# Kernel optimization log

Hardware: AMD Instinct MI355X
Metric: run time of the kernel (lower is better)

Reference implementation:

```python
import jax, jax.numpy as jnp
import numpy as np

NUM_CAPS = 10
DIM_CAPS = 16
ROUTINGS = 3


def setup_inputs() -> dict:
    key = jax.random.key(0)
    k1, k2 = jax.random.split(key)
    x = jax.random.normal(k1, (128, 1152, 512), dtype=jnp.float32)
    # glorot-uniform-ish scale for W [D_in, num_caps*dim_caps]
    limit = (6.0 / (512 + NUM_CAPS * DIM_CAPS)) ** 0.5
    W = jax.random.uniform(k2, (512, NUM_CAPS * DIM_CAPS), dtype=jnp.float32,
                           minval=-limit, maxval=limit)
    return {"x": x, "W": W}


def _squash(s, axis=-1):
    # s_norm = ||s|| + 1e-7; out = s_norm^2/(1+s_norm^2) * s/s_norm
    s_norm = jnp.linalg.norm(s, axis=axis, keepdims=True) + 1e-7
    return (s_norm ** 2) / (1.0 + s_norm ** 2) * (s / s_norm)


def reference(x, W):
    B, N, _ = x.shape
    # u_hat: [B, N, C, D]
    u_hat = jnp.matmul(x, W).reshape(B, N, NUM_CAPS, DIM_CAPS)
    b = jnp.zeros((B, N, NUM_CAPS), dtype=u_hat.dtype)
    v = None
    for i in range(ROUTINGS):
        c = jax.nn.softmax(b, axis=2)                      # [B, N, C]
        s = jnp.einsum('bnc,bncd->bcd', c, u_hat)          # [B, C, D]
        v = _squash(s)                                     # [B, C, D]
        if i < ROUTINGS - 1:
            b = b + jnp.einsum('bncd,bcd->bnc', u_hat, v)
    return v
```

## Files before the change

### kernel.cpp

```cpp
#include <hip/hip_runtime.h>

#define BB 128
#define NN 1152
#define KD 512
#define NC 10
#define ND 16
#define CD 160

typedef unsigned short ushort_t;
typedef unsigned int uint_t;
typedef short short8v __attribute__((ext_vector_type(8)));
typedef float float4v __attribute__((ext_vector_type(4)));

__device__ __forceinline__ float bf2f(ushort_t u) {
  return __uint_as_float(((uint_t)u) << 16);
}
__device__ __forceinline__ ushort_t f2bf(float f) {
  uint_t x = __float_as_uint(f);
  x += 0x7fffu + ((x >> 16) & 1u);
  return (ushort_t)(x >> 16);
}

#define BAR_LDS() do {                                   \
    __builtin_amdgcn_sched_barrier(0);                   \
    asm volatile("s_waitcnt lgkmcnt(0)" ::: "memory");   \
    __builtin_amdgcn_s_barrier();                        \
    __builtin_amdgcn_sched_barrier(0);                   \
  } while (0)

__global__ __launch_bounds__(256) void wconv(const float* __restrict__ W,
                                             ushort_t* __restrict__ Wt) {
  int idx = blockIdx.x * 256 + threadIdx.x;
  int n = idx >> 9, k = idx & 511;
  Wt[idx] = f2bf(W[(size_t)k * CD + n]);
}

__global__ __launch_bounds__(256) void gemm_mfma(
    const float* __restrict__ x, const ushort_t* __restrict__ Wt,
    ushort_t* __restrict__ uhat, float* __restrict__ partials) {
  __shared__ char smem[57344];
  __shared__ float sA[4][CD];
  const int tid = threadIdx.x;
  const int wave = tid >> 6, lane = tid & 63;
  const int lrow = lane & 15, lg = lane >> 4;
  const int row0 = blockIdx.x * 64;

  float4v acc[10];
#pragma unroll
  for (int nt = 0; nt < 10; ++nt)
#pragma unroll
    for (int r = 0; r < 4; ++r) acc[nt][r] = 0.f;

  const int arow_ = tid >> 3;
  const int as = tid & 7;
  int bsrc[5], bby[5];
#pragma unroll
  for (int i = 0; i < 5; ++i) {
    int f = tid + i * 256;
    int br = f >> 3, bs = f & 7;
    bsrc[i] = br * KD + bs * 8;
    bby[i] = ((br << 7) + (bs << 4)) ^ ((br & 7) << 4);
  }
  const int aby0 = ((arow_ << 7) + (as << 4)) ^ ((arow_ & 7) << 4);
  const int aby1 = (((arow_ + 32) << 7) + (as << 4)) ^ (((arow_ + 32) & 7) << 4);

  float4v rA[2][2];
  short8v rB[5];

  auto LOADS = [&](int ks) {
    int k0 = ks * 64;
#pragma unroll
    for (int i = 0; i < 2; ++i) {
      const float* p = x + (size_t)(row0 + arow_ + i * 32) * KD + k0 + as * 8;
      rA[i][0] = *reinterpret_cast<const float4v*>(p);
      rA[i][1] = *reinterpret_cast<const float4v*>(p + 4);
    }
#pragma unroll
    for (int i = 0; i < 5; ++i)
      rB[i] = *reinterpret_cast<const short8v*>(Wt + bsrc[i] + k0);
  };
  auto WRITES = [&](int buf) {
    char* Ab = smem + buf * 8192;
    char* Bb = smem + 16384 + buf * 20480;
#pragma unroll
    for (int i = 0; i < 2; ++i) {
      short8v pk;
#pragma unroll
      for (int e = 0; e < 4; ++e) {
        pk[e] = (short)f2bf(rA[i][0][e]);
        pk[e + 4] = (short)f2bf(rA[i][1][e]);
      }
      *reinterpret_cast<short8v*>(Ab + (i ? aby1 : aby0)) = pk;
    }
#pragma unroll
    for (int i = 0; i < 5; ++i)
      *reinterpret_cast<short8v*>(Bb + bby[i]) = rB[i];
  };

  const int arow = wave * 16 + lrow;
  LOADS(0);
  WRITES(0);
  LOADS(1);
  BAR_LDS();
  int cur = 0;
  for (int ks = 0; ks < 8; ++ks) {
    const char* Ab = smem + cur * 8192;
    const char* Bb = smem + 16384 + cur * 20480;
#pragma unroll
    for (int kk = 0; kk < 2; ++kk) {
      int abyte = ((arow << 7) + kk * 64 + lg * 16) ^ ((arow & 7) << 4);
      short8v a = *reinterpret_cast<const short8v*>(Ab + abyte);
#pragma unroll
      for (int nt = 0; nt < 10; ++nt) {
        int brow = nt * 16 + lrow;
        int bbyte = ((brow << 7) + kk * 64 + lg * 16) ^ ((brow & 7) << 4);
        short8v bfr = *reinterpret_cast<const short8v*>(Bb + bbyte);
        acc[nt] = __builtin_amdgcn_mfma_f32_16x16x32_bf16(a, bfr, acc[nt], 0, 0, 0);
      }
    }
    if (ks < 7) {
      WRITES(cur ^ 1);
      if (ks < 6) LOADS(ks + 2);
    }
    BAR_LDS();
    cur ^= 1;
  }

#pragma unroll
  for (int nt = 0; nt < 10; ++nt) {
    float p = acc[nt][0] + acc[nt][1] + acc[nt][2] + acc[nt][3];
    p += __shfl_xor(p, 16);
    p += __shfl_xor(p, 32);
    if (lg == 0) sA[wave][nt * 16 + lrow] = p;
  }

  ushort_t* Ct = reinterpret_cast<ushort_t*>(smem);
#pragma unroll
  for (int nt = 0; nt < 10; ++nt)
#pragma unroll
    for (int r = 0; r < 4; ++r) {
      int row = wave * 16 + lg * 4 + r;
      Ct[row * 168 + nt * 16 + lrow] = f2bf(acc[nt][r]);
    }
  __syncthreads();
  if (tid < CD) {
    float s = sA[0][tid] + sA[1][tid] + sA[2][tid] + sA[3][tid];
    partials[(size_t)blockIdx.x * CD + tid] = s;
  }
#pragma unroll
  for (int i = 0; i < 5; ++i) {
    int p = tid + i * 256;
    int row = p / 20, c0 = (p % 20) * 8;
    *reinterpret_cast<short8v*>(&uhat[(size_t)(row0 + row) * CD + c0]) =
        *reinterpret_cast<const short8v*>(&Ct[row * 168 + c0]);
  }
}

#define ITER_T 640
template <int ITER2>
__global__ __launch_bounds__(ITER_T) void iter_k(
    const ushort_t* __restrict__ uhat, const float* __restrict__ pg,
    const float* __restrict__ p1, float* __restrict__ pout) {
  __shared__ float bv[128][NC];
  __shared__ float wv[128][NC];
  __shared__ float sred[32][CD];
  __shared__ float sred2[4][CD];
  __shared__ float vv[CD];
  const int blk = blockIdx.x;
  const int b = blk / 9, ch = blk % 9;
  const int t = threadIdx.x;
  const int g = t / 20, q = t % 20;
  const int c = q >> 1;
  const ushort_t* ub = uhat + ((size_t)b * NN + ch * 128) * CD + q * 8;

  if (t < CD) {
    float s0 = 0.f;
#pragma unroll
    for (int cc = 0; cc < 18; ++cc) s0 += pg[((size_t)b * 18 + cc) * CD + t];
    s0 *= 0.1f;
    float ss = s0 * s0;
    ss += __shfl_xor(ss, 1); ss += __shfl_xor(ss, 2);
    ss += __shfl_xor(ss, 4); ss += __shfl_xor(ss, 8);
    float sn = sqrtf(ss) + 1e-7f;
    float v = s0 * sn / (1.f + sn * sn);
    if (ITER2) {
      float s1 = 0.f;
#pragma unroll
      for (int cc = 0; cc < 9; ++cc) s1 += p1[((size_t)b * 9 + cc) * CD + t];
      float ss1 = s1 * s1;
      ss1 += __shfl_xor(ss1, 1); ss1 += __shfl_xor(ss1, 2);
      ss1 += __shfl_xor(ss1, 4); ss1 += __shfl_xor(ss1, 8);
      float sn1 = sqrtf(ss1) + 1e-7f;
      v += s1 * sn1 / (1.f + sn1 * sn1);
    }
    vv[t] = v;
  }
  __syncthreads();

  float v0r[8];
  {
    float4v a = *reinterpret_cast<const float4v*>(&vv[q * 8]);
    float4v bb = *reinterpret_cast<const float4v*>(&vv[q * 8 + 4]);
#pragma unroll
    for (int e = 0; e < 4; ++e) { v0r[e] = a[e]; v0r[e + 4] = bb[e]; }
  }

  short8v u8[4];
#pragma unroll
  for (int it = 0; it < 4; ++it) {
    int n = g + it * 32;
    u8[it] = *reinterpret_cast<const short8v*>(ub + (size_t)n * CD);
    float p = 0.f;
#pragma unroll
    for (int e = 0; e < 8; ++e) p += bf2f((ushort_t)u8[it][e]) * v0r[e];
    p += __shfl_xor(p, 1);
    if ((q & 1) == 0) bv[n][c] = p;
  }
  __syncthreads();

  if (t < 128) {
    float e[NC];
    float bm = bv[t][0];
#pragma unroll
    for (int cc = 1; cc < NC; ++cc) bm = fmaxf(bm, bv[t][cc]);
    float Z = 0.f;
#pragma unroll
    for (int cc = 0; cc < NC; ++cc) { e[cc] = __expf(bv[t][cc] - bm); Z += e[cc]; }
    float rz = 1.f / Z;
#pragma unroll
    for (int cc = 0; cc < NC; ++cc) wv[t][cc] = e[cc] * rz;
  }
  __syncthreads();

  float a[8];
#pragma unroll
  for (int e = 0; e < 8; ++e) a[e] = 0.f;
#pragma unroll
  for (int it = 0; it < 4; ++it) {
    int n = g + it * 32;
    float w = wv[n][c];
#pragma unroll
    for (int e = 0; e < 8; ++e) a[e] += w * bf2f((ushort_t)u8[it][e]);
  }
  {
    float4v lo, hi;
#pragma unroll
    for (int e = 0; e < 4; ++e) { lo[e] = a[e]; hi[e] = a[e + 4]; }
    float4v* dst = reinterpret_cast<float4v*>(&sred[g][q * 8]);
    dst[0] = lo; dst[1] = hi;
  }
  __syncthreads();
  {
    int col = t % CD, part = t / CD;
    float s = 0.f;
#pragma unroll
    for (int g8 = 0; g8 < 8; ++g8) s += sred[part * 8 + g8][col];
    sred2[part][col] = s;
  }
  __syncthreads();
  if (t < CD) {
    pout[(size_t)blk * CD + t] =
        sred2[0][t] + sred2[1][t] + sred2[2][t] + sred2[3][t];
  }
}

__global__ __launch_bounds__(CD) void squash_out(
    const float* __restrict__ p2, float* __restrict__ outp) {
  int b = blockIdx.x, t = threadIdx.x;
  float s = 0.f;
#pragma unroll
  for (int cc = 0; cc < 9; ++cc) s += p2[((size_t)b * 9 + cc) * CD + t];
  float ss = s * s;
  ss += __shfl_xor(ss, 1); ss += __shfl_xor(ss, 2);
  ss += __shfl_xor(ss, 4); ss += __shfl_xor(ss, 8);
  float sn = sqrtf(ss) + 1e-7f;
  outp[(size_t)b * CD + t] = s * sn / (1.f + sn * sn);
}

extern "C" void kernel_launch(void* const* d_in, const int* in_sizes, int n_in,
                              void* d_out, int out_size, void* d_ws, size_t ws_size,
                              hipStream_t stream) {
  const float* x = (const float*)d_in[0];
  const float* W = (const float*)d_in[1];
  float* out = (float*)d_out;

  char* ws = (char*)d_ws;
  ushort_t* uhat = (ushort_t*)ws;
  ushort_t* Wt   = (ushort_t*)(ws + 47185920);
  float*    pg   = (float*)(ws + 47185920 + 163840);
  float*    p1   = (float*)(ws + 48824320);
  float*    p2   = (float*)(ws + 49561600);

  wconv<<<320, 256, 0, stream>>>(W, Wt);
  gemm_mfma<<<2304, 256, 0, stream>>>(x, Wt, uhat, pg);
  iter_k<0><<<1152, ITER_T, 0, stream>>>(uhat, pg, nullptr, p1);
  iter_k<1><<<1152, ITER_T, 0, stream>>>(uhat, pg, p1, p2);
  squash_out<<<BB, CD, 0, stream>>>(p2, out);
}
```

Baseline: 109.8 us.

## Halve GEMM K-tile to shrink LDS and raise occupancy

The GEMM K-step drops from 64 to 32, so each of the 16 iterations loads one A row-chunk per thread and up to three B chunks. LDS falls from about 57KB to 28KB, the swizzle is rewritten for 64-byte rows, and the row-sum scratch now reuses the main buffer. Launch bounds ask for 4 blocks per CU. The aim is more resident blocks to hide global load latency, paid for with twice as many barriers and less work between them.

```diff
diff --git a/kernel.cpp b/kernel.cpp
--- a/kernel.cpp
+++ b/kernel.cpp
@@ -35,11 +35,10 @@
   Wt[idx] = f2bf(W[(size_t)k * CD + n]);
 }
 
-__global__ __launch_bounds__(256) void gemm_mfma(
+__global__ __launch_bounds__(256, 4) void gemm_mfma(
     const float* __restrict__ x, const ushort_t* __restrict__ Wt,
     ushort_t* __restrict__ uhat, float* __restrict__ partials) {
-  __shared__ char smem[57344];
-  __shared__ float sA[4][CD];
+  __shared__ __align__(16) char smem[28672];
   const int tid = threadIdx.x;
   const int wave = tid >> 6, lane = tid & 63;
   const int lrow = lane & 15, lg = lane >> 4;
@@ -51,87 +50,79 @@
 #pragma unroll
     for (int r = 0; r < 4; ++r) acc[nt][r] = 0.f;
 
-  const int arow_ = tid >> 3;
-  const int as = tid & 7;
-  int bsrc[5], bby[5];
-#pragma unroll
-  for (int i = 0; i < 5; ++i) {
+  const int arow_ = tid >> 2;
+  const int as = tid & 3;
+  const int aby = (arow_ << 6) + ((as ^ ((arow_ >> 1) & 3)) << 4);
+  int bsrc[3], bby[3];
+#pragma unroll
+  for (int i = 0; i < 3; ++i) {
     int f = tid + i * 256;
-    int br = f >> 3, bs = f & 7;
+    int br = f >> 2, bs = f & 3;
     bsrc[i] = br * KD + bs * 8;
-    bby[i] = ((br << 7) + (bs << 4)) ^ ((br & 7) << 4);
-  }
-  const int aby0 = ((arow_ << 7) + (as << 4)) ^ ((arow_ & 7) << 4);
-  const int aby1 = (((arow_ + 32) << 7) + (as << 4)) ^ (((arow_ + 32) & 7) << 4);
-
-  float4v rA[2][2];
-  short8v rB[5];
+    bby[i] = (br << 6) + ((bs ^ ((br >> 1) & 3)) << 4);
+  }
+  const bool b2ok = (tid + 512) < 640;
+
+  float4v rA[2];
+  short8v rB[3];
 
   auto LOADS = [&](int ks) {
-    int k0 = ks * 64;
-#pragma unroll
-    for (int i = 0; i < 2; ++i) {
-      const float* p = x + (size_t)(row0 + arow_ + i * 32) * KD + k0 + as * 8;
-      rA[i][0] = *reinterpret_cast<const float4v*>(p);
-      rA[i][1] = *reinterpret_cast<const float4v*>(p + 4);
-    }
-#pragma unroll
-    for (int i = 0; i < 5; ++i)
-      rB[i] = *reinterpret_cast<const short8v*>(Wt + bsrc[i] + k0);
+    int k0 = ks * 32;
+    const float* p = x + (size_t)(row0 + arow_) * KD + k0 + as * 8;
+    rA[0] = *reinterpret_cast<const float4v*>(p);
+    rA[1] = *reinterpret_cast<const float4v*>(p + 4);
+    rB[0] = *reinterpret_cast<const short8v*>(Wt + bsrc[0] + k0);
+    rB[1] = *reinterpret_cast<const short8v*>(Wt + bsrc[1] + k0);
+    if (b2ok) rB[2] = *reinterpret_cast<const short8v*>(Wt + bsrc[2] + k0);
   };
   auto WRITES = [&](int buf) {
-    char* Ab = smem + buf * 8192;
-    char* Bb = smem + 16384 + buf * 20480;
-#pragma unroll
-    for (int i = 0; i < 2; ++i) {
-      short8v pk;
-#pragma unroll
-      for (int e = 0; e < 4; ++e) {
-        pk[e] = (short)f2bf(rA[i][0][e]);
-        pk[e + 4] = (short)f2bf(rA[i][1][e]);
-      }
-      *reinterpret_cast<short8v*>(Ab + (i ? aby1 : aby0)) = pk;
-    }
-#pragma unroll
-    for (int i = 0; i < 5; ++i)
-      *reinterpret_cast<short8v*>(Bb + bby[i]) = rB[i];
+    char* Ab = smem + buf * 4096;
+    char* Bb = smem + 8192 + buf * 10240;
+    short8v pk;
+#pragma unroll
+    for (int e = 0; e < 4; ++e) {
+      pk[e] = (short)f2bf(rA[0][e]);
+      pk[e + 4] = (short)f2bf(rA[1][e]);
+    }
+    *reinterpret_cast<short8v*>(Ab + aby) = pk;
+    *reinterpret_cast<short8v*>(Bb + bby[0]) = rB[0];
+    *reinterpret_cast<short8v*>(Bb + bby[1]) = rB[1];
+    if (b2ok) *reinterpret_cast<short8v*>(Bb + bby[2]) = rB[2];
   };
 
   const int arow = wave * 16 + lrow;
+  const int afrag_by = (arow << 6) + ((lg ^ ((arow >> 1) & 3)) << 4);
   LOADS(0);
   WRITES(0);
   LOADS(1);
   BAR_LDS();
   int cur = 0;
-  for (int ks = 0; ks < 8; ++ks) {
-    const char* Ab = smem + cur * 8192;
-    const char* Bb = smem + 16384 + cur * 20480;
-#pragma unroll
-    for (int kk = 0; kk < 2; ++kk) {
-      int abyte = ((arow << 7) + kk * 64 + lg * 16) ^ ((arow & 7) << 4);
-      short8v a = *reinterpret_cast<const short8v*>(Ab + abyte);
-#pragma unroll
-      for (int nt = 0; nt < 10; ++nt) {
-        int brow = nt * 16 + lrow;
-        int bbyte = ((brow << 7) + kk * 64 + lg * 16) ^ ((brow & 7) << 4);
-        short8v bfr = *reinterpret_cast<const short8v*>(Bb + bbyte);
-        acc[nt] = __builtin_amdgcn_mfma_f32_16x16x32_bf16(a, bfr, acc[nt], 0, 0, 0);
-      }
-    }
-    if (ks < 7) {
+  for (int ks = 0; ks < 16; ++ks) {
+    const char* Ab = smem + cur * 4096;
+    const char* Bb = smem + 8192 + cur * 10240;
+    short8v a = *reinterpret_cast<const short8v*>(Ab + afrag_by);
+#pragma unroll
+    for (int nt = 0; nt < 10; ++nt) {
+      int brow = nt * 16 + lrow;
+      int bbyte = (brow << 6) + ((lg ^ ((brow >> 1) & 3)) << 4);
+      short8v bfr = *reinterpret_cast<const short8v*>(Bb + bbyte);
+      acc[nt] = __builtin_amdgcn_mfma_f32_16x16x32_bf16(a, bfr, acc[nt], 0, 0, 0);
+    }
+    if (ks < 15) {
       WRITES(cur ^ 1);
-      if (ks < 6) LOADS(ks + 2);
+      if (ks < 14) LOADS(ks + 2);
     }
     BAR_LDS();
     cur ^= 1;
   }
 
+  float* sAf = reinterpret_cast<float*>(smem + 24576);
 #pragma unroll
   for (int nt = 0; nt < 10; ++nt) {
     float p = acc[nt][0] + acc[nt][1] + acc[nt][2] + acc[nt][3];
     p += __shfl_xor(p, 16);
     p += __shfl_xor(p, 32);
-    if (lg == 0) sA[wave][nt * 16 + lrow] = p;
+    if (lg == 0) sAf[wave * CD + nt * 16 + lrow] = p;
   }
 
   ushort_t* Ct = reinterpret_cast<ushort_t*>(smem);
@@ -144,7 +135,7 @@
     }
   __syncthreads();
   if (tid < CD) {
-    float s = sA[0][tid] + sA[1][tid] + sA[2][tid] + sA[3][tid];
+    float s = sAf[tid] + sAf[CD + tid] + sAf[2 * CD + tid] + sAf[3 * CD + tid];
     partials[(size_t)blockIdx.x * CD + tid] = s;
   }
 #pragma unroll
```

Result: slower. 123.3 us (+12.3%).

## Double GEMM row tile to 128 with 512-thread blocks sharing W tile

Applied to the files above, without the earlier changes.

The GEMM block now covers 128 rows of x with 8 waves instead of 64 rows with 4, so each staged W tile in LDS is reused by twice as many rows. This halves the grid and halves the per-block partial sums, and the iteration kernel now reduces 9 partials per batch instead of 18. LDS per block grows to about 77KB, which can limit how many blocks fit per CU, and the larger block may change latency hiding.

```diff
diff --git a/kernel.cpp b/kernel.cpp
--- a/kernel.cpp
+++ b/kernel.cpp
@@ -35,15 +35,14 @@
   Wt[idx] = f2bf(W[(size_t)k * CD + n]);
 }
 
-__global__ __launch_bounds__(256) void gemm_mfma(
+__global__ __launch_bounds__(512, 4) void gemm_mfma(
     const float* __restrict__ x, const ushort_t* __restrict__ Wt,
     ushort_t* __restrict__ uhat, float* __restrict__ partials) {
-  __shared__ char smem[57344];
-  __shared__ float sA[4][CD];
+  __shared__ __align__(16) char smem[78848];
   const int tid = threadIdx.x;
-  const int wave = tid >> 6, lane = tid & 63;
+  const int wid = tid >> 6, lane = tid & 63;
   const int lrow = lane & 15, lg = lane >> 4;
-  const int row0 = blockIdx.x * 64;
+  const int row0 = blockIdx.x * 128;
 
   float4v acc[10];
 #pragma unroll
@@ -51,37 +50,39 @@
 #pragma unroll
     for (int r = 0; r < 4; ++r) acc[nt][r] = 0.f;
 
-  const int arow_ = tid >> 3;
-  const int as = tid & 7;
-  int bsrc[5], bby[5];
-#pragma unroll
-  for (int i = 0; i < 5; ++i) {
-    int f = tid + i * 256;
-    int br = f >> 3, bs = f & 7;
+  const int ar0 = tid >> 3;
+  const int akq = tid & 7;
+  const int aby0 = (ar0 << 7) + ((akq << 4) ^ ((ar0 & 7) << 4));
+  const int ar1 = ar0 + 64;
+  const int aby1 = (ar1 << 7) + ((akq << 4) ^ ((ar1 & 7) << 4));
+  int bsrc[3], bby[3];
+#pragma unroll
+  for (int i = 0; i < 3; ++i) {
+    int f = tid + i * 512;
+    int br = (f >> 3) % 160, bs = f & 7;
     bsrc[i] = br * KD + bs * 8;
-    bby[i] = ((br << 7) + (bs << 4)) ^ ((br & 7) << 4);
-  }
-  const int aby0 = ((arow_ << 7) + (as << 4)) ^ ((arow_ & 7) << 4);
-  const int aby1 = (((arow_ + 32) << 7) + (as << 4)) ^ (((arow_ + 32) & 7) << 4);
+    bby[i] = (br << 7) + ((bs << 4) ^ ((br & 7) << 4));
+  }
+  const bool b2ok = (tid + 1024) < 1280;
 
   float4v rA[2][2];
-  short8v rB[5];
+  short8v rB[3];
 
   auto LOADS = [&](int ks) {
     int k0 = ks * 64;
-#pragma unroll
-    for (int i = 0; i < 2; ++i) {
-      const float* p = x + (size_t)(row0 + arow_ + i * 32) * KD + k0 + as * 8;
-      rA[i][0] = *reinterpret_cast<const float4v*>(p);
-      rA[i][1] = *reinterpret_cast<const float4v*>(p + 4);
-    }
-#pragma unroll
-    for (int i = 0; i < 5; ++i)
-      rB[i] = *reinterpret_cast<const short8v*>(Wt + bsrc[i] + k0);
+    const float* p0 = x + (size_t)(row0 + ar0) * KD + k0 + akq * 8;
+    const float* p1 = x + (size_t)(row0 + ar1) * KD + k0 + akq * 8;
+    rA[0][0] = *reinterpret_cast<const float4v*>(p0);
+    rA[0][1] = *reinterpret_cast<const float4v*>(p0 + 4);
+    rA[1][0] = *reinterpret_cast<const float4v*>(p1);
+    rA[1][1] = *reinterpret_cast<const float4v*>(p1 + 4);
+    rB[0] = *reinterpret_cast<const short8v*>(Wt + bsrc[0] + k0);
+    rB[1] = *reinterpret_cast<const short8v*>(Wt + bsrc[1] + k0);
+    if (b2ok) rB[2] = *reinterpret_cast<const short8v*>(Wt + bsrc[2] + k0);
   };
   auto WRITES = [&](int buf) {
-    char* Ab = smem + buf * 8192;
-    char* Bb = smem + 16384 + buf * 20480;
+    char* Ab = smem + buf * 16384;
+    char* Bb = smem + 32768 + buf * 20480;
 #pragma unroll
     for (int i = 0; i < 2; ++i) {
       short8v pk;
@@ -92,20 +93,20 @@
       }
       *reinterpret_cast<short8v*>(Ab + (i ? aby1 : aby0)) = pk;
     }
-#pragma unroll
-    for (int i = 0; i < 5; ++i)
-      *reinterpret_cast<short8v*>(Bb + bby[i]) = rB[i];
+    *reinterpret_cast<short8v*>(Bb + bby[0]) = rB[0];
+    *reinterpret_cast<short8v*>(Bb + bby[1]) = rB[1];
+    if (b2ok) *reinterpret_cast<short8v*>(Bb + bby[2]) = rB[2];
   };
 
-  const int arow = wave * 16 + lrow;
+  const int arow = wid * 16 + lrow;
   LOADS(0);
   WRITES(0);
   LOADS(1);
   BAR_LDS();
   int cur = 0;
   for (int ks = 0; ks < 8; ++ks) {
-    const char* Ab = smem + cur * 8192;
-    const char* Bb = smem + 16384 + cur * 20480;
+    const char* Ab = smem + cur * 16384;
+    const char* Bb = smem + 32768 + cur * 20480;
 #pragma unroll
     for (int kk = 0; kk < 2; ++kk) {
       int abyte = ((arow << 7) + kk * 64 + lg * 16) ^ ((arow & 7) << 4);
@@ -126,12 +127,13 @@
     cur ^= 1;
   }
 
+  float* sAf = reinterpret_cast<float*>(smem + 73728);
 #pragma unroll
   for (int nt = 0; nt < 10; ++nt) {
     float p = acc[nt][0] + acc[nt][1] + acc[nt][2] + acc[nt][3];
     p += __shfl_xor(p, 16);
     p += __shfl_xor(p, 32);
-    if (lg == 0) sA[wave][nt * 16 + lrow] = p;
+    if (lg == 0) sAf[wid * CD + nt * 16 + lrow] = p;
   }
 
   ushort_t* Ct = reinterpret_cast<ushort_t*>(smem);
@@ -139,17 +141,19 @@
   for (int nt = 0; nt < 10; ++nt)
 #pragma unroll
     for (int r = 0; r < 4; ++r) {
-      int row = wave * 16 + lg * 4 + r;
+      int row = wid * 16 + lg * 4 + r;
       Ct[row * 168 + nt * 16 + lrow] = f2bf(acc[nt][r]);
     }
   __syncthreads();
   if (tid < CD) {
-    float s = sA[0][tid] + sA[1][tid] + sA[2][tid] + sA[3][tid];
+    float s = 0.f;
+#pragma unroll
+    for (int w = 0; w < 8; ++w) s += sAf[w * CD + tid];
     partials[(size_t)blockIdx.x * CD + tid] = s;
   }
 #pragma unroll
   for (int i = 0; i < 5; ++i) {
-    int p = tid + i * 256;
+    int p = tid + i * 512;
     int row = p / 20, c0 = (p % 20) * 8;
     *reinterpret_cast<short8v*>(&uhat[(size_t)(row0 + row) * CD + c0]) =
         *reinterpret_cast<const short8v*>(&Ct[row * 168 + c0]);
@@ -176,7 +180,7 @@
   if (t < CD) {
     float s0 = 0.f;
 #pragma unroll
-    for (int cc = 0; cc < 18; ++cc) s0 += pg[((size_t)b * 18 + cc) * CD + t];
+    for (int cc = 0; cc < 9; ++cc) s0 += pg[((size_t)b * 9 + cc) * CD + t];
     s0 *= 0.1f;
     float ss = s0 * s0;
     ss += __shfl_xor(ss, 1); ss += __shfl_xor(ss, 2);
@@ -287,12 +291,12 @@
   char* ws = (char*)d_ws;
   ushort_t* uhat = (ushort_t*)ws;
   ushort_t* Wt   = (ushort_t*)(ws + 47185920);
-  float*    pg   = (float*)(ws + 47185920 + 163840);
-  float*    p1   = (float*)(ws + 48824320);
-  float*    p2   = (float*)(ws + 49561600);
+  float*    pg   = (float*)(ws + 47349760);
+  float*    p1   = (float*)(ws + 48087040);
+  float*    p2   = (float*)(ws + 48824320);
 
   wconv<<<320, 256, 0, stream>>>(W, Wt);
-  gemm_mfma<<<2304, 256, 0, stream>>>(x, Wt, uhat, pg);
+  gemm_mfma<<<1152, 512, 0, stream>>>(x, Wt, uhat, pg);
   iter_k<0><<<1152, ITER_T, 0, stream>>>(uhat, pg, nullptr, p1);
   iter_k<1><<<1152, ITER_T, 0, stream>>>(uhat, pg, p1, p2);
   squash_out<<<BB, CD, 0, stream>>>(p2, out);
```

Measured after the change: 126.3 us. 1.15x slower.

## Switch GEMM to 128-row tiles using 32x32x16 bf16 MFMA

Applied to the files above, without the earlier changes.

The projection GEMM now processes 128 rows per block instead of 64, with each wave owning a 32-row strip and using the 32x32x16 bf16 MFMA across five 32-column tiles. This halves the grid and the per-row reloading of the W tile into shared memory, and reduces LDS fragment reads per MFMA. The partial-sum buffer shrinks to 9 chunks per batch, and downstream reads and workspace offsets are adjusted to match. Shared memory grows to 72KB and the kernel requests two blocks per CU, which costs occupancy and register headroom for the larger accumulators.

```diff
diff --git a/kernel.cpp b/kernel.cpp
--- a/kernel.cpp
+++ b/kernel.cpp
@@ -11,6 +11,7 @@
 typedef unsigned int uint_t;
 typedef short short8v __attribute__((ext_vector_type(8)));
 typedef float float4v __attribute__((ext_vector_type(4)));
+typedef float float16v __attribute__((ext_vector_type(16)));
 
 __device__ __forceinline__ float bf2f(ushort_t u) {
   return __uint_as_float(((uint_t)u) << 16);
@@ -35,43 +36,47 @@
   Wt[idx] = f2bf(W[(size_t)k * CD + n]);
 }
 
-__global__ __launch_bounds__(256) void gemm_mfma(
+__global__ __launch_bounds__(256, 2) void gemm_mfma(
     const float* __restrict__ x, const ushort_t* __restrict__ Wt,
     ushort_t* __restrict__ uhat, float* __restrict__ partials) {
-  __shared__ char smem[57344];
-  __shared__ float sA[4][CD];
+  __shared__ __align__(16) char smem[73728];
   const int tid = threadIdx.x;
-  const int wave = tid >> 6, lane = tid & 63;
-  const int lrow = lane & 15, lg = lane >> 4;
-  const int row0 = blockIdx.x * 64;
-
-  float4v acc[10];
-#pragma unroll
-  for (int nt = 0; nt < 10; ++nt)
-#pragma unroll
-    for (int r = 0; r < 4; ++r) acc[nt][r] = 0.f;
-
+  const int wid = tid >> 6, lane = tid & 63;
+  const int l31 = lane & 31, lh = lane >> 5;
+  const int row0 = blockIdx.x * 128;
+
+  float16v acc[5];
+#pragma unroll
+  for (int nt = 0; nt < 5; ++nt)
+#pragma unroll
+    for (int r = 0; r < 16; ++r) acc[nt][r] = 0.f;
+
+  int aby[4];
+#pragma unroll
+  for (int i = 0; i < 4; ++i) {
+    int f = tid + i * 256;
+    int ar = f >> 3, s = f & 7;
+    aby[i] = (ar << 7) + ((s ^ (ar & 7)) << 4);
+  }
   const int arow_ = tid >> 3;
-  const int as = tid & 7;
+  const int akq = tid & 7;
   int bsrc[5], bby[5];
 #pragma unroll
   for (int i = 0; i < 5; ++i) {
     int f = tid + i * 256;
     int br = f >> 3, bs = f & 7;
     bsrc[i] = br * KD + bs * 8;
-    bby[i] = ((br << 7) + (bs << 4)) ^ ((br & 7) << 4);
-  }
-  const int aby0 = ((arow_ << 7) + (as << 4)) ^ ((arow_ & 7) << 4);
-  const int aby1 = (((arow_ + 32) << 7) + (as << 4)) ^ (((arow_ + 32) & 7) << 4);
-
-  float4v rA[2][2];
+    bby[i] = (br << 7) + ((bs ^ (br & 7)) << 4);
+  }
+
+  float4v rA[4][2];
   short8v rB[5];
 
   auto LOADS = [&](int ks) {
     int k0 = ks * 64;
 #pragma unroll
-    for (int i = 0; i < 2; ++i) {
-      const float* p = x + (size_t)(row0 + arow_ + i * 32) * KD + k0 + as * 8;
+    for (int i = 0; i < 4; ++i) {
+      const float* p = x + (size_t)(row0 + arow_ + i * 32) * KD + k0 + akq * 8;
       rA[i][0] = *reinterpret_cast<const float4v*>(p);
       rA[i][1] = *reinterpret_cast<const float4v*>(p + 4);
     }
@@ -80,42 +85,44 @@
       rB[i] = *reinterpret_cast<const short8v*>(Wt + bsrc[i] + k0);
   };
   auto WRITES = [&](int buf) {
-    char* Ab = smem + buf * 8192;
-    char* Bb = smem + 16384 + buf * 20480;
-#pragma unroll
-    for (int i = 0; i < 2; ++i) {
+    char* Ab = smem + buf * 16384;
+    char* Bb = smem + 32768 + buf * 20480;
+#pragma unroll
+    for (int i = 0; i < 4; ++i) {
       short8v pk;
 #pragma unroll
       for (int e = 0; e < 4; ++e) {
         pk[e] = (short)f2bf(rA[i][0][e]);
         pk[e + 4] = (short)f2bf(rA[i][1][e]);
       }
-      *reinterpret_cast<short8v*>(Ab + (i ? aby1 : aby0)) = pk;
+      *reinterpret_cast<short8v*>(Ab + aby[i]) = pk;
     }
 #pragma unroll
     for (int i = 0; i < 5; ++i)
       *reinterpret_cast<short8v*>(Bb + bby[i]) = rB[i];
   };
 
-  const int arow = wave * 16 + lrow;
+  const int arow = wid * 32 + l31;
+  const int arx = (arow & 7);
   LOADS(0);
   WRITES(0);
   LOADS(1);
   BAR_LDS();
   int cur = 0;
   for (int ks = 0; ks < 8; ++ks) {
-    const char* Ab = smem + cur * 8192;
-    const char* Bb = smem + 16384 + cur * 20480;
-#pragma unroll
-    for (int kk = 0; kk < 2; ++kk) {
-      int abyte = ((arow << 7) + kk * 64 + lg * 16) ^ ((arow & 7) << 4);
-      short8v a = *reinterpret_cast<const short8v*>(Ab + abyte);
-#pragma unroll
-      for (int nt = 0; nt < 10; ++nt) {
-        int brow = nt * 16 + lrow;
-        int bbyte = ((brow << 7) + kk * 64 + lg * 16) ^ ((brow & 7) << 4);
-        short8v bfr = *reinterpret_cast<const short8v*>(Bb + bbyte);
-        acc[nt] = __builtin_amdgcn_mfma_f32_16x16x32_bf16(a, bfr, acc[nt], 0, 0, 0);
+    const char* Ab = smem + cur * 16384;
+    const char* Bb = smem + 32768 + cur * 20480;
+#pragma unroll
+    for (int ss = 0; ss < 4; ++ss) {
+      int slot = ss * 2 + lh;
+      short8v a = *reinterpret_cast<const short8v*>(
+          Ab + (arow << 7) + ((slot ^ arx) << 4));
+#pragma unroll
+      for (int nt = 0; nt < 5; ++nt) {
+        int brow = nt * 32 + l31;
+        short8v bfr = *reinterpret_cast<const short8v*>(
+            Bb + (brow << 7) + ((slot ^ (brow & 7)) << 4));
+        acc[nt] = __builtin_amdgcn_mfma_f32_32x32x16_bf16(a, bfr, acc[nt], 0, 0, 0);
       }
     }
     if (ks < 7) {
@@ -126,29 +133,31 @@
     cur ^= 1;
   }
 
-#pragma unroll
-  for (int nt = 0; nt < 10; ++nt) {
-    float p = acc[nt][0] + acc[nt][1] + acc[nt][2] + acc[nt][3];
-    p += __shfl_xor(p, 16);
+  float* sAf = reinterpret_cast<float*>(smem + 43008);
+#pragma unroll
+  for (int nt = 0; nt < 5; ++nt) {
+    float p = 0.f;
+#pragma unroll
+    for (int r = 0; r < 16; ++r) p += acc[nt][r];
     p += __shfl_xor(p, 32);
-    if (lg == 0) sA[wave][nt * 16 + lrow] = p;
+    if (lh == 0) sAf[wid * CD + nt * 32 + l31] = p;
   }
 
   ushort_t* Ct = reinterpret_cast<ushort_t*>(smem);
 #pragma unroll
-  for (int nt = 0; nt < 10; ++nt)
-#pragma unroll
-    for (int r = 0; r < 4; ++r) {
-      int row = wave * 16 + lg * 4 + r;
-      Ct[row * 168 + nt * 16 + lrow] = f2bf(acc[nt][r]);
+  for (int nt = 0; nt < 5; ++nt)
+#pragma unroll
+    for (int r = 0; r < 16; ++r) {
+      int row = wid * 32 + (r & 3) + 8 * (r >> 2) + 4 * lh;
+      Ct[row * 168 + nt * 32 + l31] = f2bf(acc[nt][r]);
     }
   __syncthreads();
   if (tid < CD) {
-    float s = sA[0][tid] + sA[1][tid] + sA[2][tid] + sA[3][tid];
+    float s = sAf[tid] + sAf[CD + tid] + sAf[2 * CD + tid] + sAf[3 * CD + tid];
     partials[(size_t)blockIdx.x * CD + tid] = s;
   }
 #pragma unroll
-  for (int i = 0; i < 5; ++i) {
+  for (int i = 0; i < 10; ++i) {
     int p = tid + i * 256;
     int row = p / 20, c0 = (p % 20) * 8;
     *reinterpret_cast<short8v*>(&uhat[(size_t)(row0 + row) * CD + c0]) =
@@ -176,7 +185,7 @@
   if (t < CD) {
     float s0 = 0.f;
 #pragma unroll
-    for (int cc = 0; cc < 18; ++cc) s0 += pg[((size_t)b * 18 + cc) * CD + t];
+    for (int cc = 0; cc < 9; ++cc) s0 += pg[((size_t)b * 9 + cc) * CD + t];
     s0 *= 0.1f;
     float ss = s0 * s0;
     ss += __shfl_xor(ss, 1); ss += __shfl_xor(ss, 2);
@@ -287,12 +296,12 @@
   char* ws = (char*)d_ws;
   ushort_t* uhat = (ushort_t*)ws;
   ushort_t* Wt   = (ushort_t*)(ws + 47185920);
-  float*    pg   = (float*)(ws + 47185920 + 163840);
-  float*    p1   = (float*)(ws + 48824320);
-  float*    p2   = (float*)(ws + 49561600);
+  float*    pg   = (float*)(ws + 47349760);
+  float*    p1   = (float*)(ws + 48087040);
+  float*    p2   = (float*)(ws + 48824320);
 
   wconv<<<320, 256, 0, stream>>>(W, Wt);
-  gemm_mfma<<<2304, 256, 0, stream>>>(x, Wt, uhat, pg);
+  gemm_mfma<<<1152, 256, 0, stream>>>(x, Wt, uhat, pg);
   iter_k<0><<<1152, ITER_T, 0, stream>>>(uhat, pg, nullptr, p1);
   iter_k<1><<<1152, ITER_T, 0, stream>>>(uhat, pg, p1, p2);
   squash_out<<<BB, CD, 0, stream>>>(p2, out);
```

Measured after the change: 103.1 us. 1.06x faster.
